# Kernel tuning notes

Measured on AMD Instinct MI355X. Metric: run time of the kernel, lower is better.

The kernel has to match this reference:

```python
import jax, jax.numpy as jnp
import numpy as np

P = 2_000_000   # total gathered points (N1+N2+... after pillar grouping)
C_IN = 10       # mlps[0]: point feats + pillar-center offsets
C_OUT = 64      # mlps[1]
M = 200_000     # number of non-empty pillars (pillar_indices.shape[0])
BN_EPS = 1e-3


def setup_inputs() -> dict:
    key = jax.random.key(0)
    k0, k1, k2, k3, k4 = jax.random.split(key, 5)
    return {
        "group_features": jax.random.normal(k0, (P, C_IN), dtype=jnp.float32),
        "pillar_set_indices": jax.random.randint(k1, (P,), 0, M, dtype=jnp.int32),
        "num_pillars": M,
        # Linear(bias=False) weight, xavier-ish scale; stored (C_IN, C_OUT) so fwd is x @ W
        "W": jax.random.normal(k2, (C_IN, C_OUT), dtype=jnp.float32) * np.float32(1.0 / np.sqrt(C_IN)),
        "gamma": jnp.ones((C_OUT,), dtype=jnp.float32),
        "beta": jnp.zeros((C_OUT,), dtype=jnp.float32),
        "running_mean": jax.random.normal(k3, (C_OUT,), dtype=jnp.float32) * 0.1,
        "running_var": jax.random.uniform(k4, (C_OUT,), dtype=jnp.float32, minval=0.5, maxval=1.5),
    }


def reference(group_features, pillar_set_indices, num_pillars, W, gamma, beta, running_mean, running_var):
    # shared MLP: Linear(bias=False) -> BatchNorm1d(eval, eps=1e-3) -> ReLU
    h = group_features @ W                                   # (P, C_OUT)
    inv_std = gamma * jax.lax.rsqrt(running_var + BN_EPS)    # fold BN scale
    h = jax.nn.relu(h * inv_std + (beta - running_mean * inv_std))
    # scatter_max segment pooling into pillars; empty pillars -> 0 (ReLU output >= 0)
    pooled = jax.ops.segment_max(h, pillar_set_indices, num_segments=num_pillars)
    pillar_features = jnp.maximum(pooled, jnp.float32(0.0))  # (M, C_OUT)
    return pillar_features
```

## Files before the change

### kernel.cpp

```cpp
#include <hip/hip_runtime.h>


#define C_IN   10
#define C_OUT  64
#define BPILL  100
#define MAXNBP 2048
#define NREG   8
#define SBLK   1024
#define SCHUNK 8192
#define PPT    (SCHUNK / SBLK)
#define PBLK   512
#define TRASH  100
#define SENT   ((unsigned)TRASH << 24)

typedef _Float16 half8  __attribute__((ext_vector_type(8)));
typedef float    f32x4  __attribute__((ext_vector_type(4)));
typedef float    f32x4a __attribute__((ext_vector_type(4), aligned(8)));

__device__ __attribute__((noinline))
void fallback_point(int p, int m, const float* gf, const float* W,
                    const float* gamma, const float* beta,
                    const float* rmean, const float* rvar,
                    float* out, int* ovf) {
    atomicExch(ovf, 1);
    const float* x = gf + (size_t)p * C_IN;
    unsigned* o = (unsigned*)out + (size_t)m * C_OUT;
#pragma clang loop unroll(disable)
    for (int c = 0; c < C_OUT; ++c) {
        float is = gamma[c] * rsqrtf(rvar[c] + 1e-3f);
        float bb = fmaf(-rmean[c], is, beta[c]);
        float d = 0.f;
        for (int k = 0; k < C_IN; ++k) d = fmaf(x[k], W[k * C_OUT + c], d);
        atomicMax(o + c, __float_as_uint(fmaxf(fmaf(d, is, bb), 0.f)));
    }
}

__global__ __launch_bounds__(SBLK)
void k_scatter(const int* __restrict__ idx,
               const float* __restrict__ gf,
               const float* __restrict__ W,
               const float* __restrict__ gamma,
               const float* __restrict__ beta,
               const float* __restrict__ rmean,
               const float* __restrict__ rvar,
               int* __restrict__ cnt, int* __restrict__ ovf,
               unsigned* __restrict__ tok,
               float* __restrict__ out,
               int P, int NBpad, int CAPR) {
    __shared__ int lh[MAXNBP];
    __shared__ int rbase[MAXNBP];
    const int t = threadIdx.x;
    const int r = blockIdx.x & (NREG - 1);

    for (int b = t; b < NBpad; b += SBLK) lh[b] = 0;
    __syncthreads();

    const int base = blockIdx.x * SCHUNK;
    int mm[PPT], rk[PPT];
#pragma unroll
    for (int i = 0; i < PPT; ++i) {
        int p = base + i * SBLK + t;
        mm[i] = (p < P) ? idx[p] : -1;
        rk[i] = (mm[i] >= 0) ? atomicAdd(&lh[mm[i] / BPILL], 1) : 0;
    }
    __syncthreads();

    int* crow = cnt + (size_t)r * NBpad;
    for (int b = t; b < NBpad; b += SBLK) {
        int h = lh[b];
        rbase[b] = h ? atomicAdd(&crow[b], h) : 0;
    }
    __syncthreads();

#pragma unroll
    for (int i = 0; i < PPT; ++i) {
        if (mm[i] < 0) continue;
        int p = base + i * SBLK + t;
        int b = mm[i] / BPILL;
        int ml = mm[i] - b * BPILL;
        int slot = rbase[b] + rk[i];
        if (slot < CAPR) {
            tok[((size_t)b * NREG + r) * CAPR + slot] =
                (unsigned)p | ((unsigned)ml << 24);
        } else {
            fallback_point(p, mm[i], gf, W, gamma, beta, rmean, rvar, out, ovf);
        }
    }
}

__global__ __launch_bounds__(PBLK, 8)
void k_pool(const float* __restrict__ gf,
            const unsigned* __restrict__ tok,
            const int* __restrict__ cnt,
            const int* __restrict__ ovf,
            const float* __restrict__ W,
            const float* __restrict__ gamma,
            const float* __restrict__ beta,
            const float* __restrict__ rmean,
            const float* __restrict__ rvar,
            float* __restrict__ out, int M, int NBpad, int CAPR) {
    __shared__ unsigned int acc[(BPILL + 1) * 65];
    const int t = threadIdx.x;
    const int lane = t & 63;
    const int wv = t >> 6;
    const int n = lane & 15;
    const int q = lane >> 4;

    for (int i = t; i < (BPILL + 1) * 65; i += PBLK) acc[i] = 0u;

    half8 bfrag[4];
    float inv[4], bia[4];
#pragma unroll
    for (int tt = 0; tt < 4; ++tt) {
        int c = tt * 16 + n;
#pragma unroll
        for (int j = 0; j < 8; ++j) {
            int k = q * 8 + j;
            bfrag[tt][j] = (k < C_IN) ? (_Float16)W[k * C_OUT + c] : (_Float16)0.f;
        }
        float is = gamma[c] * rsqrtf(rvar[c] + 1e-3f);
        inv[tt] = is;
        bia[tt] = fmaf(-rmean[c], is, beta[c]);
    }
    __syncthreads();

    const int blk = blockIdx.x;
    const int cn = min(cnt[(size_t)wv * NBpad + blk], CAPR);
    const unsigned* src0 = tok + ((size_t)blk * NREG + wv) * CAPR;

    unsigned vcur = (lane < cn) ? src0[lane] : SENT;

    for (int rb = 0; rb < cn; rb += 64) {
        unsigned vnext = (rb + 64 + lane < cn) ? src0[rb + 64 + lane] : SENT;

        const char* rowp = (const char*)gf + (size_t)(vcur & 0xFFFFFFu) * 40;
        f32x4a xa = *(const f32x4a*)rowp;
        f32x4a xb = *(const f32x4a*)(rowp + 16);
        float2 xc = *(const float2*)(rowp + 32);
        int u0 = __builtin_bit_cast(int, __builtin_amdgcn_cvt_pkrtz(xa.x, xa.y));
        int u1 = __builtin_bit_cast(int, __builtin_amdgcn_cvt_pkrtz(xa.z, xa.w));
        int u2 = __builtin_bit_cast(int, __builtin_amdgcn_cvt_pkrtz(xb.x, xb.y));
        int u3 = __builtin_bit_cast(int, __builtin_amdgcn_cvt_pkrtz(xb.z, xb.w));
        int u4 = __builtin_bit_cast(int, __builtin_amdgcn_cvt_pkrtz(xc.x, xc.y));

        const int ng = min(4, ((cn - rb) + 15) >> 4);
#pragma unroll
        for (int g = 0; g < 4; ++g) {
            if (g >= ng) break;
            const int sl = (g << 4) + n;
            int b0 = __shfl(u0, sl, 64);
            int b1 = __shfl(u1, sl, 64);
            int b2 = __shfl(u2, sl, 64);
            int b3 = __shfl(u3, sl, 64);
            int b4 = __shfl(u4, sl, 64);
            int4 a32;
            a32.x = (q == 0) ? b0 : ((q == 1) ? b4 : 0);
            a32.y = (q == 0) ? b1 : 0;
            a32.z = (q == 0) ? b2 : 0;
            a32.w = (q == 0) ? b3 : 0;
            half8 a = __builtin_bit_cast(half8, a32);
            f32x4 z = {0.f, 0.f, 0.f, 0.f};
            f32x4 d0 = __builtin_amdgcn_mfma_f32_16x16x32_f16(a, bfrag[0], z, 0, 0, 0);
            f32x4 d1 = __builtin_amdgcn_mfma_f32_16x16x32_f16(a, bfrag[1], z, 0, 0, 0);
            f32x4 d2 = __builtin_amdgcn_mfma_f32_16x16x32_f16(a, bfrag[2], z, 0, 0, 0);
            f32x4 d3 = __builtin_amdgcn_mfma_f32_16x16x32_f16(a, bfrag[3], z, 0, 0, 0);
#pragma unroll
            for (int r = 0; r < 4; ++r) {
                int mlr = __shfl((int)vcur, (g << 4) + (q << 2) + r, 64);
                int abase = (int)(((unsigned)mlr) >> 24) * 65 + n;
                float h0 = fmaxf(fmaf(d0[r], inv[0], bia[0]), 0.f);
                float h1 = fmaxf(fmaf(d1[r], inv[1], bia[1]), 0.f);
                float h2 = fmaxf(fmaf(d2[r], inv[2], bia[2]), 0.f);
                float h3 = fmaxf(fmaf(d3[r], inv[3], bia[3]), 0.f);
                atomicMax(&acc[abase +  0], __float_as_uint(h0));
                atomicMax(&acc[abase + 16], __float_as_uint(h1));
                atomicMax(&acc[abase + 32], __float_as_uint(h2));
                atomicMax(&acc[abase + 48], __float_as_uint(h3));
            }
        }
        vcur = vnext;
    }
    __syncthreads();

    const int anyovf = ovf[0];
    const int mbase = blk * BPILL;
#pragma unroll
    for (int i = 0; i < (BPILL * C_OUT + PBLK - 1) / PBLK; ++i) {
        int wdx = i * PBLK + t;
        if (wdx >= BPILL * C_OUT) break;
        int row = wdx >> 6, c = wdx & 63;
        int m = mbase + row;
        if (m < M) {
            unsigned uv = acc[row * 65 + c];
            if (anyovf) atomicMax((unsigned*)out + (size_t)m * C_OUT + c, uv);
            else        out[(size_t)m * C_OUT + c] = __uint_as_float(uv);
        }
    }
}

extern "C" void kernel_launch(void* const* d_in, const int* in_sizes, int n_in,
                              void* d_out, int out_size, void* d_ws, size_t ws_size,
                              hipStream_t stream) {
    const float* gf    = (const float*)d_in[0];
    const int*   idx   = (const int*)  d_in[1];
    const float* W     = (const float*)d_in[3];
    const float* gamma = (const float*)d_in[4];
    const float* beta  = (const float*)d_in[5];
    const float* rmean = (const float*)d_in[6];
    const float* rvar  = (const float*)d_in[7];
    float*       out   = (float*)d_out;

    const int P  = in_sizes[0] / C_IN;
    const int M  = out_size / C_OUT;
    const int NB    = (M + BPILL - 1) / BPILL;
    const int NBpad = (NB + 32) & ~31;
    const int E     = NREG * NBpad;
    const int NSB   = (P + SCHUNK - 1) / SCHUNK;

    char* ws = (char*)d_ws;
    auto align256 = [](size_t x) { return (x + 255) & ~(size_t)255; };
    int* cnt = (int*)ws;  ws += align256((size_t)E * 4);
    int* ovf = (int*)ws;  ws += 256;
    unsigned* tok = (unsigned*)ws;

    int CAPR = 256;
    size_t fixed = (size_t)((char*)tok - (char*)cnt);
    size_t avail = (ws_size > fixed) ? ws_size - fixed : 0;
    while (CAPR > 128 && (size_t)E * CAPR * 4 > avail) CAPR -= 64;

    hipMemsetAsync(cnt, 0, fixed, stream);

    k_scatter<<<NSB, SBLK, 0, stream>>>(idx, gf, W, gamma, beta, rmean, rvar,
                                        cnt, ovf, tok, out, P, NBpad, CAPR);
    k_pool   <<<NB,  PBLK, 0, stream>>>(gf, tok, cnt, ovf, W, gamma, beta,
                                        rmean, rvar, out, M, NBpad, CAPR);
}
```

Measured before the change: 213.2 us.

## Stage scatter tokens in shared memory sorted by bucket for coalesced writes

```diff
diff --git a/kernel.cpp b/kernel.cpp
--- a/kernel.cpp
+++ b/kernel.cpp
@@ -12,6 +12,7 @@
 #define PBLK   512
 #define TRASH  100
 #define SENT   ((unsigned)TRASH << 24)
+#define SKIP   0xFFFFFFFFu
 
 typedef _Float16 half8  __attribute__((ext_vector_type(8)));
 typedef float    f32x4  __attribute__((ext_vector_type(4)));
@@ -49,13 +50,16 @@
                int P, int NBpad, int CAPR) {
     __shared__ int lh[MAXNBP];
     __shared__ int rbase[MAXNBP];
+    __shared__ unsigned stok[SCHUNK];
+    __shared__ unsigned sdst[SCHUNK];
     const int t = threadIdx.x;
     const int r = blockIdx.x & (NREG - 1);
 
-    for (int b = t; b < NBpad; b += SBLK) lh[b] = 0;
+    for (int b = t; b < MAXNBP; b += SBLK) lh[b] = 0;
     __syncthreads();
 
     const int base = blockIdx.x * SCHUNK;
+    const int tot  = min(SCHUNK, P - base);
     int mm[PPT], rk[PPT];
 #pragma unroll
     for (int i = 0; i < PPT; ++i) {
@@ -65,11 +69,27 @@
     }
     __syncthreads();
 
+    int* tmp = (int*)stok;
+    const int b0i = 2 * t, b1i = 2 * t + 1;
+    const int s0 = (b0i < NBpad) ? lh[b0i] : 0;
+    const int s1 = (b1i < NBpad) ? lh[b1i] : 0;
+    tmp[t] = s0 + s1;
     int* crow = cnt + (size_t)r * NBpad;
     for (int b = t; b < NBpad; b += SBLK) {
         int h = lh[b];
         rbase[b] = h ? atomicAdd(&crow[b], h) : 0;
     }
+    __syncthreads();
+
+#pragma unroll
+    for (int off = 1; off < SBLK; off <<= 1) {
+        int x = (t >= off) ? tmp[t - off] : 0;
+        __syncthreads(); tmp[t] += x; __syncthreads();
+    }
+    const int ex = tmp[t] - (s0 + s1);
+    __syncthreads();
+    if (b0i < NBpad) lh[b0i] = ex;
+    if (b1i < NBpad) lh[b1i] = ex + s0;
     __syncthreads();
 
 #pragma unroll
@@ -78,12 +98,24 @@
         int p = base + i * SBLK + t;
         int b = mm[i] / BPILL;
         int ml = mm[i] - b * BPILL;
+        int pos  = lh[b] + rk[i];
         int slot = rbase[b] + rk[i];
+        stok[pos] = (unsigned)p | ((unsigned)ml << 24);
         if (slot < CAPR) {
-            tok[((size_t)b * NREG + r) * CAPR + slot] =
-                (unsigned)p | ((unsigned)ml << 24);
+            sdst[pos] = (unsigned)(((size_t)b * NREG + r) * CAPR + slot);
         } else {
+            sdst[pos] = SKIP;
             fallback_point(p, mm[i], gf, W, gamma, beta, rmean, rvar, out, ovf);
+        }
+    }
+    __syncthreads();
+
+#pragma unroll
+    for (int k = 0; k < PPT; ++k) {
+        int j = k * SBLK + t;
+        if (j < tot) {
+            unsigned d = sdst[j];
+            if (d != SKIP) tok[d] = stok[j];
         }
     }
 }
```

Result: no change. 209.9 us (-1.5%).
